# Performance work log

Hardware: AMD Instinct MI355X
Metric: run time of the kernel (lower is better)

Reference implementation:

```python
import jax, jax.numpy as jnp
import numpy as np

DIM_IN, DIM_KEY, HEADS = 1024, 64, 16
B, S = 4, 2048

def setup_inputs() -> dict:
    key = jax.random.key(0)
    ks = jax.random.split(key, 7)
    scale_in = 1.0 / np.sqrt(DIM_IN)
    scale_hd = 1.0 / np.sqrt(HEADS * DIM_KEY)
    return {
        'q_in': jax.random.normal(ks[0], (B, S, DIM_IN), dtype=jnp.float32),
        'k_in': jax.random.normal(ks[1], (B, S, DIM_IN), dtype=jnp.float32),
        'v_in': jax.random.normal(ks[2], (B, S, DIM_IN), dtype=jnp.float32),
        'Wq': jax.random.normal(ks[3], (DIM_IN, HEADS * DIM_KEY), dtype=jnp.float32) * scale_in,
        'Wk': jax.random.normal(ks[4], (DIM_IN, HEADS * DIM_KEY), dtype=jnp.float32) * scale_in,
        'Wv': jax.random.normal(ks[5], (DIM_IN, HEADS * DIM_KEY), dtype=jnp.float32) * scale_in,
        'Wo': jax.random.normal(ks[6], (HEADS * DIM_KEY, DIM_IN), dtype=jnp.float32) * scale_hd,
    }

def reference(q_in, k_in, v_in, Wq, Wk, Wv, Wo):
    b, s, _ = q_in.shape
    def proj(x, W):
        # [B,S,D] @ [D,H*dk] -> [B,H,S,dk]
        return (x @ W).reshape(b, s, HEADS, DIM_KEY).transpose(0, 2, 1, 3)
    q, k, v = proj(q_in, Wq), proj(k_in, Wk), proj(v_in, Wv)
    # scores: [B,H,S,S]; original scales AFTER matmul by 1/sqrt(dim_key)
    score = jnp.einsum('bhqd,bhkd->bhqk', q, k) / jnp.sqrt(jnp.float32(DIM_KEY))
    p = jax.nn.softmax(score, axis=-1)  # dropout is identity in eval mode
    out = jnp.einsum('bhqk,bhkd->bhqd', p, v)
    out = out.transpose(0, 2, 1, 3).reshape(b, s, HEADS * DIM_KEY)
    return out @ Wo
```

## Files before the change

kernel.cpp:

```cpp
#include <hip/hip_runtime.h>
#include <hip/hip_bf16.h>

#define DIN   1024
#define HEADS 16
#define DK    64
#define BATCH 4
#define SEQ   2048
#define MROWS (BATCH*SEQ)
#define HD    (HEADS*DK)

typedef unsigned short u16;
typedef unsigned int   u32;
typedef __attribute__((ext_vector_type(8))) short v8s;
typedef __attribute__((ext_vector_type(4))) float v4f;

__device__ __forceinline__ u16 f2bf(float x) {
  union { float f; u32 u; } v; v.f = x;
  u32 r = v.u + 0x7FFFu + ((v.u >> 16) & 1u);
  return (u16)(r >> 16);
}
__device__ __forceinline__ int cvtpk(float lo, float hi) {
  int r;
  asm("v_cvt_pk_bf16_f32 %0, %1, %2" : "=v"(r) : "v"(lo), "v"(hi));
  return r;
}
__device__ __forceinline__ float max3f(float a, float b, float c) {
  float r;
  asm("v_max3_f32 %0, %1, %2, %3" : "=v"(r) : "v"(a), "v"(b), "v"(c));
  return r;
}
__device__ __forceinline__ void gload16(const void* g, void* l) {
  __builtin_amdgcn_global_load_lds(
      (__attribute__((address_space(1))) void*)(uintptr_t)(g),
      (__attribute__((address_space(3))) void*)(uintptr_t)(l), 16, 0, 0);
}
__device__ __forceinline__ v8s lds_read_swz(const u16* base, int row, int unit) {
  return *(const v8s*)((const char*)base + (row << 7) + (((unit) ^ (row & 7)) << 4));
}

__global__ __launch_bounds__(256) void wtrans4_kernel(
    const float* __restrict__ w0, const float* __restrict__ w1,
    const float* __restrict__ w2, const float* __restrict__ w3,
    u16* __restrict__ o0, u16* __restrict__ o1,
    u16* __restrict__ o2, u16* __restrict__ o3) {
  __shared__ float tile[64][65];
  const float* in = blockIdx.z == 0 ? w0 : blockIdx.z == 1 ? w1 : blockIdx.z == 2 ? w2 : w3;
  u16* out = blockIdx.z == 0 ? o0 : blockIdx.z == 1 ? o1 : blockIdx.z == 2 ? o2 : o3;
  int bx = blockIdx.x * 64;
  int by = blockIdx.y * 64;
  for (int i = threadIdx.x; i < 64 * 64; i += 256) {
    int r = i >> 6, c = i & 63;
    tile[r][c] = in[(size_t)(by + r) * DIN + bx + c];
  }
  __syncthreads();
  for (int i = threadIdx.x; i < 64 * 64; i += 256) {
    int r = i >> 6, c = i & 63;
    out[(size_t)(bx + r) * DIN + by + c] = f2bf(tile[c][r]);
  }
}

__global__ __launch_bounds__(256) void gemm_qkv_kernel(
    const float* __restrict__ q_in, const float* __restrict__ k_in,
    const float* __restrict__ v_in, const u16* __restrict__ Wtq,
    const u16* __restrict__ Wtk, const u16* __restrict__ Wtv,
    u16* __restrict__ Qb, u16* __restrict__ Kb, u16* __restrict__ VtB) {
  __shared__ u16 A_lds[2][128 * 32];
  __shared__ u16 B_lds[2][128 * 32];
  const int which = blockIdx.x >> 9;
  const float* Ain = which == 0 ? q_in : which == 1 ? k_in : v_in;
  const u16* Bt = which == 0 ? Wtq : which == 1 ? Wtk : Wtv;
  u16* Cout = which == 0 ? Qb : which == 1 ? Kb : VtB;

  const int tid = threadIdx.x;
  const int lane = tid & 63;
  const int wv = tid >> 6;
  const int wm = wv & 1, wn = wv >> 1;
  const int bid = blockIdx.x & 511;
  const int swz = (bid & 7) * 64 + (bid >> 3);
  const int m0 = (swz >> 3) * 128;
  const int n0 = (swz & 7) * 128;
  const int l15 = lane & 15;
  const int k8 = (lane >> 4) * 8;

  const float* gaf = Ain + (size_t)(m0 + wv * 16 + (lane >> 2)) * DIN + (lane & 3) * 8;
  const u16* gb = Bt + (size_t)(n0 + wv * 16 + (lane >> 2)) * DIN + (lane & 3) * 8;
  u16* la0 = &A_lds[0][wv * 512 + (lane & 63) * 8];
  u16* la1 = &A_lds[1][wv * 512 + (lane & 63) * 8];

  v4f acc[4][4];
#pragma unroll
  for (int i = 0; i < 4; i++)
#pragma unroll
    for (int j = 0; j < 4; j++) acc[i][j] = (v4f)0.f;

  float4 af0, af1, af2, af3;

#define A_GLOAD(ks)                                                   \
  do {                                                                \
    af0 = ((const float4*)(gaf + (ks) * 32))[0];                      \
    af1 = ((const float4*)(gaf + (ks) * 32))[1];                      \
    af2 = ((const float4*)(gaf + (size_t)64 * DIN + (ks) * 32))[0];   \
    af3 = ((const float4*)(gaf + (size_t)64 * DIN + (ks) * 32))[1];   \
  } while (0)
#define A_DSWRITE(b)                                                  \
  do {                                                                \
    int4 w0 = {cvtpk(af0.x, af0.y), cvtpk(af0.z, af0.w),              \
               cvtpk(af1.x, af1.y), cvtpk(af1.z, af1.w)};             \
    int4 w1 = {cvtpk(af2.x, af2.y), cvtpk(af2.z, af2.w),              \
               cvtpk(af3.x, af3.y), cvtpk(af3.z, af3.w)};             \
    *(int4*)((b) ? la1 : la0) = w0;                                   \
    *(int4*)(((b) ? la1 : la0) + 2048) = w1;                          \
  } while (0)
#define B_STAGE(ks, b)                                                \
  do {                                                                \
    gload16(gb + (ks) * 32, &B_lds[b][wv * 512]);                     \
    gload16(gb + (size_t)64 * DIN + (ks) * 32, &B_lds[b][wv * 512 + 2048]); \
  } while (0)

  A_GLOAD(0);
  A_DSWRITE(0);
  B_STAGE(0, 0);
  __syncthreads();

  for (int ks = 0; ks < 32; ++ks) {
    const int buf = ks & 1;
    v8s a[4], b[4];
#pragma unroll
    for (int mi = 0; mi < 4; mi++)
      a[mi] = *(const v8s*)&A_lds[buf][(wm * 64 + mi * 16 + l15) * 32 + k8];
#pragma unroll
    for (int ni = 0; ni < 4; ni++)
      b[ni] = *(const v8s*)&B_lds[buf][(wn * 64 + ni * 16 + l15) * 32 + k8];
    if (ks < 31) {
      A_GLOAD(ks + 1);
      B_STAGE(ks + 1, buf ^ 1);
    }
    __builtin_amdgcn_s_setprio(1);
#pragma unroll
    for (int mi = 0; mi < 4; mi++)
#pragma unroll
      for (int ni = 0; ni < 4; ni++)
        acc[mi][ni] = __builtin_amdgcn_mfma_f32_16x16x32_bf16(a[mi], b[ni], acc[mi][ni], 0, 0, 0);
    __builtin_amdgcn_s_setprio(0);
    if (ks < 31) A_DSWRITE(buf ^ 1);
    __syncthreads();
  }
#undef A_GLOAD
#undef A_DSWRITE
#undef B_STAGE

  const int grp = lane >> 4;
#pragma unroll
  for (int mi = 0; mi < 4; mi++) {
#pragma unroll
    for (int ni = 0; ni < 4; ni++) {
      int row = m0 + wm * 64 + mi * 16 + grp * 4;
      int col = n0 + wn * 64 + ni * 16 + l15;
      int w01 = cvtpk(acc[mi][ni][0], acc[mi][ni][1]);
      int w23 = cvtpk(acc[mi][ni][2], acc[mi][ni][3]);
      if (which < 2) {
        u16 h[4] = {(u16)w01, (u16)(w01 >> 16), (u16)w23, (u16)(w23 >> 16)};
#pragma unroll
        for (int r = 0; r < 4; r++) {
          int bb = (row + r) >> 11, ss = (row + r) & 2047;
          int hh = col >> 6, dd = col & 63;
          Cout[((((size_t)bb * HEADS + hh) * SEQ + ss) << 6) + dd] = h[r];
        }
      } else {
        int bb = row >> 11, ss = row & 2047;
        int hh = col >> 6, dd = col & 63;
        int2 w = {w01, w23};
        *(int2*)&Cout[((size_t)(bb * HEADS + hh) * DK + dd) * SEQ + ss] = w;
      }
    }
  }
}

__global__ __launch_bounds__(256) void gemm_o_kernel(const u16* __restrict__ A,
                                                     const u16* __restrict__ Bt,
                                                     float* __restrict__ Cout) {
  __shared__ u16 A_lds[2][128 * 32];
  __shared__ u16 B_lds[2][128 * 32];
  const int tid = threadIdx.x;
  const int lane = tid & 63;
  const int wv = tid >> 6;
  const int wm = wv & 1, wn = wv >> 1;
  const int bid = blockIdx.x;
  const int swz = (bid & 7) * 64 + (bid >> 3);
  const int m0 = (swz >> 3) * 128;
  const int n0 = (swz & 7) * 128;
  const int l15 = lane & 15;
  const int k8 = (lane >> 4) * 8;

  const u16* ga = A + (size_t)(m0 + wv * 16 + (lane >> 2)) * DIN + (lane & 3) * 8;
  const u16* gb = Bt + (size_t)(n0 + wv * 16 + (lane >> 2)) * DIN + (lane & 3) * 8;

  v4f acc[4][4];
#pragma unroll
  for (int i = 0; i < 4; i++)
#pragma unroll
    for (int j = 0; j < 4; j++) acc[i][j] = (v4f)0.f;

#define G_STAGE(ks, b)                                              \
  do {                                                              \
    gload16(ga + (ks) * 32, &A_lds[b][wv * 512]);                   \
    gload16(ga + (size_t)64 * DIN + (ks) * 32, &A_lds[b][wv * 512 + 2048]); \
    gload16(gb + (ks) * 32, &B_lds[b][wv * 512]);                   \
    gload16(gb + (size_t)64 * DIN + (ks) * 32, &B_lds[b][wv * 512 + 2048]); \
  } while (0)

  G_STAGE(0, 0);
  __syncthreads();
  for (int ks = 0; ks < 32; ++ks) {
    const int buf = ks & 1;
    v8s a[4], b[4];
#pragma unroll
    for (int mi = 0; mi < 4; mi++)
      a[mi] = *(const v8s*)&A_lds[buf][(wm * 64 + mi * 16 + l15) * 32 + k8];
#pragma unroll
    for (int ni = 0; ni < 4; ni++)
      b[ni] = *(const v8s*)&B_lds[buf][(wn * 64 + ni * 16 + l15) * 32 + k8];
    if (ks < 31) G_STAGE(ks + 1, buf ^ 1);
    __builtin_amdgcn_s_setprio(1);
#pragma unroll
    for (int mi = 0; mi < 4; mi++)
#pragma unroll
      for (int ni = 0; ni < 4; ni++)
        acc[mi][ni] = __builtin_amdgcn_mfma_f32_16x16x32_bf16(a[mi], b[ni], acc[mi][ni], 0, 0, 0);
    __builtin_amdgcn_s_setprio(0);
    __syncthreads();
  }
#undef G_STAGE

  const int grp = lane >> 4;
#pragma unroll
  for (int mi = 0; mi < 4; mi++) {
#pragma unroll
    for (int ni = 0; ni < 4; ni++) {
#pragma unroll
      for (int r = 0; r < 4; r++) {
        int row = m0 + wm * 64 + mi * 16 + grp * 4 + r;
        int col = n0 + wn * 64 + ni * 16 + l15;
        Cout[(size_t)row * HD + col] = acc[mi][ni][r];
      }
    }
  }
}

__global__ __launch_bounds__(512) void attn_kernel(const u16* __restrict__ Q,
                                                   const u16* __restrict__ Kmat,
                                                   const u16* __restrict__ Vt,
                                                   u16* __restrict__ AO) {
  __shared__ u16 K_lds[64 * 64];
  __shared__ u16 V_lds[64 * 64];
  __shared__ u16 P_lds[8][16][72];

  const int tid = threadIdx.x;
  const int lane = tid & 63;
  const int wv = tid >> 6;
  const int l15 = lane & 15;
  const int grp = lane >> 4;
  const int k8 = grp * 8;

  const int bid = blockIdx.x;
  const int swz = (bid & 7) * 128 + (bid >> 3);
  const int bh = swz >> 4;
  const int qt = swz & 15;
  const size_t base = (size_t)bh * SEQ * DK;

  v8s qf[2];
  {
    const int q = qt * 128 + wv * 16 + l15;
    const u16* qp = Q + base + (size_t)q * DK;
    qf[0] = *(const v8s*)(qp + k8);
    qf[1] = *(const v8s*)(qp + 32 + k8);
    const float SCL = 0.125f * 1.44269504f;
#pragma unroll
    for (int j = 0; j < 8; j++) {
      union { float f; u32 u; } a;
      a.u = ((u32)(u16)qf[0][j]) << 16; a.f *= SCL; qf[0][j] = (short)f2bf(a.f);
      a.u = ((u32)(u16)qf[1][j]) << 16; a.f *= SCL; qf[1][j] = (short)f2bf(a.f);
    }
  }

  v8s ones;
#pragma unroll
  for (int j = 0; j < 8; j++) ones[j] = (short)0x3F80;

  float mrow = -1e30f;
  v4f oacc[5];
#pragma unroll
  for (int db = 0; db < 5; db++) oacc[db] = (v4f)0.f;

  const int srow = tid >> 3;
  const int au = tid & 7;
  const int sw = srow & 7;
  const u16* kp_base = Kmat + base + (size_t)srow * DK + au * 8;
  const u16* vp_base = Vt + base + (size_t)srow * SEQ + au * 8;
  u16* krow = &K_lds[srow << 6];
  u16* vrow = &V_lds[srow << 6];

  int4 kr0, vr0;
#define A_LOAD(t)                                                  \
  do {                                                             \
    kr0 = *(const int4*)(kp_base + (size_t)(t) * 64 * DK);         \
    vr0 = *(const int4*)(vp_base + (t) * 64);                      \
  } while (0)
#define A_WRITE()                                                  \
  do {                                                             \
    *(int4*)((char*)krow + ((au ^ sw) << 4)) = kr0;                \
    *(int4*)((char*)vrow + ((au ^ sw) << 4)) = vr0;                \
  } while (0)

  A_LOAD(0);

  for (int t = 0; t < SEQ / 64; ++t) {
    __syncthreads();
    A_WRITE();
    __syncthreads();
    if (t + 1 < SEQ / 64) A_LOAD(t + 1);

    v4f sacc[4];
#pragma unroll
    for (int kb = 0; kb < 4; kb++) sacc[kb] = (v4f)0.f;
    __builtin_amdgcn_s_setprio(1);
#pragma unroll
    for (int ks = 0; ks < 2; ks++)
#pragma unroll
      for (int kb = 0; kb < 4; kb++) {
        v8s kf = lds_read_swz(K_lds, kb * 16 + l15, ks * 4 + grp);
        sacc[kb] = __builtin_amdgcn_mfma_f32_16x16x32_bf16(kf, qf[ks], sacc[kb], 0, 0, 0);
      }
    __builtin_amdgcn_s_setprio(0);

    float m1 = max3f(sacc[0][0], sacc[0][1], sacc[0][2]);
    float m2 = max3f(sacc[0][3], sacc[1][0], sacc[1][1]);
    float m3 = max3f(sacc[1][2], sacc[1][3], sacc[2][0]);
    float m4 = max3f(sacc[2][1], sacc[2][2], sacc[2][3]);
    float m5 = max3f(sacc[3][0], sacc[3][1], sacc[3][2]);
    float mx = fmaxf(max3f(m1, m2, m3), max3f(m4, m5, sacc[3][3]));
    mx = fmaxf(mx, __shfl_xor(mx, 16));
    mx = fmaxf(mx, __shfl_xor(mx, 32));
    if (__any(mx - mrow > 8.f)) {
      float mnew = fmaxf(mrow, mx);
      float fac = __builtin_amdgcn_exp2f(mrow - mnew);
#pragma unroll
      for (int db = 0; db < 5; db++) oacc[db] *= fac;
      mrow = mnew;
    }
    float p[4][4];
#pragma unroll
    for (int kb = 0; kb < 4; kb++)
#pragma unroll
      for (int r = 0; r < 4; r++)
        p[kb][r] = __builtin_amdgcn_exp2f(sacc[kb][r] - mrow);

#pragma unroll
    for (int kb = 0; kb < 4; kb++) {
      int2 w;
      w.x = cvtpk(p[kb][0], p[kb][1]);
      w.y = cvtpk(p[kb][2], p[kb][3]);
      *(int2*)&P_lds[wv][l15][kb * 16 + grp * 4] = w;
    }
    asm volatile("s_waitcnt lgkmcnt(0)" ::: "memory");

    __builtin_amdgcn_s_setprio(1);
#pragma unroll
    for (int ks = 0; ks < 2; ks++) {
      v8s pf = *(const v8s*)&P_lds[wv][l15][ks * 32 + k8];
#pragma unroll
      for (int db = 0; db < 4; db++) {
        v8s vf = lds_read_swz(V_lds, db * 16 + l15, ks * 4 + grp);
        oacc[db] = __builtin_amdgcn_mfma_f32_16x16x32_bf16(vf, pf, oacc[db], 0, 0, 0);
      }
      oacc[4] = __builtin_amdgcn_mfma_f32_16x16x32_bf16(ones, pf, oacc[4], 0, 0, 0);
    }
    __builtin_amdgcn_s_setprio(0);
  }
#undef A_LOAD
#undef A_WRITE

  const int bb = bh >> 4, hh = bh & 15;
  const int q = qt * 128 + wv * 16 + l15;
  const float inv = 1.0f / oacc[4][0];
  const size_t rowbase = ((size_t)bb * SEQ + q) * HD + hh * DK;
#pragma unroll
  for (int db = 0; db < 4; db++) {
    int2 w;
    w.x = cvtpk(oacc[db][0] * inv, oacc[db][1] * inv);
    w.y = cvtpk(oacc[db][2] * inv, oacc[db][3] * inv);
    *(int2*)&AO[rowbase + db * 16 + grp * 4] = w;
  }
}

extern "C" void kernel_launch(void* const* d_in, const int* in_sizes, int n_in,
                              void* d_out, int out_size, void* d_ws, size_t ws_size,
                              hipStream_t stream) {
  const float* q_in = (const float*)d_in[0];
  const float* k_in = (const float*)d_in[1];
  const float* v_in = (const float*)d_in[2];
  const float* Wq = (const float*)d_in[3];
  const float* Wk = (const float*)d_in[4];
  const float* Wv = (const float*)d_in[5];
  const float* Wo = (const float*)d_in[6];
  float* out = (float*)d_out;

  u16* ws = (u16*)d_ws;
  const size_t M1 = (size_t)1 << 20;
  u16* Wtq = ws;
  u16* Wtk = Wtq + M1;
  u16* Wtv = Wtk + M1;
  u16* Wto = Wtv + M1;
  u16* Qb = Wto + M1;
  u16* Kb = Qb + (size_t)MROWS * HD;
  u16* VtB = Kb + (size_t)MROWS * HD;
  u16* AO = VtB + (size_t)MROWS * HD;

  dim3 tb(256);
  wtrans4_kernel<<<dim3(16, 16, 4), tb, 0, stream>>>(Wq, Wk, Wv, Wo, Wtq, Wtk, Wtv, Wto);

  gemm_qkv_kernel<<<dim3(1536), tb, 0, stream>>>(q_in, k_in, v_in,
                                                 Wtq, Wtk, Wtv, Qb, Kb, VtB);

  attn_kernel<<<dim3(1024), dim3(512), 0, stream>>>(Qb, Kb, VtB, AO);

  gemm_o_kernel<<<dim3(512), tb, 0, stream>>>(AO, Wto, out);
}
```

Baseline: 199.8 us.

## Switch attention to 32x32x16 MFMA with register-resident P via permlane32 swap

The attention kernel now uses 4 waves (256 threads) per block, each owning 32 query rows, and computes S and O with 32x32x16 bf16 MFMAs instead of 16x16x32. The P tile no longer goes through LDS: it is converted to bf16 and rearranged in registers with v_permlane32_swap so it can feed the PV MFMA directly. The softmax row sum is accumulated in registers rather than with an extra ones-vector MFMA. The aim is to cut LDS round-trips and extra MFMAs per tile, at the cost of more registers per wave and fewer waves per block for hiding latency.

```diff
diff --git a/kernel.cpp b/kernel.cpp
--- a/kernel.cpp
+++ b/kernel.cpp
@@ -13,6 +13,7 @@
 typedef unsigned int   u32;
 typedef __attribute__((ext_vector_type(8))) short v8s;
 typedef __attribute__((ext_vector_type(4))) float v4f;
+typedef __attribute__((ext_vector_type(16))) float v16f;
 
 __device__ __forceinline__ u16 f2bf(float x) {
   union { float f; u32 u; } v; v.f = x;
@@ -247,20 +248,18 @@
   }
 }
 
-__global__ __launch_bounds__(512) void attn_kernel(const u16* __restrict__ Q,
+__global__ __launch_bounds__(256) void attn_kernel(const u16* __restrict__ Q,
                                                    const u16* __restrict__ Kmat,
                                                    const u16* __restrict__ Vt,
                                                    u16* __restrict__ AO) {
   __shared__ u16 K_lds[64 * 64];
   __shared__ u16 V_lds[64 * 64];
-  __shared__ u16 P_lds[8][16][72];
 
   const int tid = threadIdx.x;
   const int lane = tid & 63;
   const int wv = tid >> 6;
-  const int l15 = lane & 15;
-  const int grp = lane >> 4;
-  const int k8 = grp * 8;
+  const int l31 = lane & 31;
+  const int h = lane >> 5;
 
   const int bid = blockIdx.x;
   const int swz = (bid & 7) * 128 + (bid >> 3);
@@ -268,48 +267,51 @@
   const int qt = swz & 15;
   const size_t base = (size_t)bh * SEQ * DK;
 
-  v8s qf[2];
+  v8s qf[4];
   {
-    const int q = qt * 128 + wv * 16 + l15;
-    const u16* qp = Q + base + (size_t)q * DK;
-    qf[0] = *(const v8s*)(qp + k8);
-    qf[1] = *(const v8s*)(qp + 32 + k8);
+    const int q = qt * 128 + wv * 32 + l31;
+    const u16* qp = Q + base + (size_t)q * DK + h * 8;
     const float SCL = 0.125f * 1.44269504f;
 #pragma unroll
-    for (int j = 0; j < 8; j++) {
-      union { float f; u32 u; } a;
-      a.u = ((u32)(u16)qf[0][j]) << 16; a.f *= SCL; qf[0][j] = (short)f2bf(a.f);
-      a.u = ((u32)(u16)qf[1][j]) << 16; a.f *= SCL; qf[1][j] = (short)f2bf(a.f);
-    }
-  }
-
-  v8s ones;
-#pragma unroll
-  for (int j = 0; j < 8; j++) ones[j] = (short)0x3F80;
-
-  float mrow = -1e30f;
-  v4f oacc[5];
-#pragma unroll
-  for (int db = 0; db < 5; db++) oacc[db] = (v4f)0.f;
-
-  const int srow = tid >> 3;
-  const int au = tid & 7;
+    for (int ks = 0; ks < 4; ks++) {
+      qf[ks] = *(const v8s*)(qp + ks * 16);
+#pragma unroll
+      for (int j = 0; j < 8; j++) {
+        union { float f; u32 u; } a;
+        a.u = ((u32)(u16)qf[ks][j]) << 16; a.f *= SCL; qf[ks][j] = (short)f2bf(a.f);
+      }
+    }
+  }
+
+  float mrow = -1e30f, lrow = 0.f;
+  v16f oacc[2];
+  oacc[0] = (v16f)0.f;
+  oacc[1] = (v16f)0.f;
+
+  const int srow = tid >> 2;
+  const int a3 = tid & 3;
   const int sw = srow & 7;
-  const u16* kp_base = Kmat + base + (size_t)srow * DK + au * 8;
-  const u16* vp_base = Vt + base + (size_t)srow * SEQ + au * 8;
+  const u16* kp_base = Kmat + base + (size_t)srow * DK + a3 * 16;
+  const u16* vp_base = Vt + base + (size_t)srow * SEQ + a3 * 16;
   u16* krow = &K_lds[srow << 6];
   u16* vrow = &V_lds[srow << 6];
 
-  int4 kr0, vr0;
+  int4 kr0, kr1, vr0, vr1;
 #define A_LOAD(t)                                                  \
   do {                                                             \
-    kr0 = *(const int4*)(kp_base + (size_t)(t) * 64 * DK);         \
-    vr0 = *(const int4*)(vp_base + (t) * 64);                      \
+    const u16* kp = kp_base + (size_t)(t) * 64 * DK;               \
+    const u16* vp = vp_base + (t) * 64;                            \
+    kr0 = ((const int4*)kp)[0];                                    \
+    kr1 = ((const int4*)kp)[1];                                    \
+    vr0 = ((const int4*)vp)[0];                                    \
+    vr1 = ((const int4*)vp)[1];                                    \
   } while (0)
 #define A_WRITE()                                                  \
   do {                                                             \
-    *(int4*)((char*)krow + ((au ^ sw) << 4)) = kr0;                \
-    *(int4*)((char*)vrow + ((au ^ sw) << 4)) = vr0;                \
+    *(int4*)((char*)krow + (((2 * a3 + 0) ^ sw) << 4)) = kr0;      \
+    *(int4*)((char*)krow + (((2 * a3 + 1) ^ sw) << 4)) = kr1;      \
+    *(int4*)((char*)vrow + (((2 * a3 + 0) ^ sw) << 4)) = vr0;      \
+    *(int4*)((char*)vrow + (((2 * a3 + 1) ^ sw) << 4)) = vr1;      \
   } while (0)
 
   A_LOAD(0);
@@ -320,77 +322,95 @@
     __syncthreads();
     if (t + 1 < SEQ / 64) A_LOAD(t + 1);
 
-    v4f sacc[4];
-#pragma unroll
-    for (int kb = 0; kb < 4; kb++) sacc[kb] = (v4f)0.f;
+    v16f sacc[2];
+    sacc[0] = (v16f)0.f;
+    sacc[1] = (v16f)0.f;
     __builtin_amdgcn_s_setprio(1);
 #pragma unroll
-    for (int ks = 0; ks < 2; ks++)
-#pragma unroll
-      for (int kb = 0; kb < 4; kb++) {
-        v8s kf = lds_read_swz(K_lds, kb * 16 + l15, ks * 4 + grp);
-        sacc[kb] = __builtin_amdgcn_mfma_f32_16x16x32_bf16(kf, qf[ks], sacc[kb], 0, 0, 0);
+    for (int ks = 0; ks < 4; ks++)
+#pragma unroll
+      for (int kb = 0; kb < 2; kb++) {
+        v8s kf = lds_read_swz(K_lds, kb * 32 + l31, ks * 2 + h);
+        sacc[kb] = __builtin_amdgcn_mfma_f32_32x32x16_bf16(kf, qf[ks], sacc[kb], 0, 0, 0);
       }
     __builtin_amdgcn_s_setprio(0);
 
-    float m1 = max3f(sacc[0][0], sacc[0][1], sacc[0][2]);
-    float m2 = max3f(sacc[0][3], sacc[1][0], sacc[1][1]);
-    float m3 = max3f(sacc[1][2], sacc[1][3], sacc[2][0]);
-    float m4 = max3f(sacc[2][1], sacc[2][2], sacc[2][3]);
-    float m5 = max3f(sacc[3][0], sacc[3][1], sacc[3][2]);
-    float mx = fmaxf(max3f(m1, m2, m3), max3f(m4, m5, sacc[3][3]));
-    mx = fmaxf(mx, __shfl_xor(mx, 16));
+    float a0 = max3f(sacc[0][0], sacc[0][1], sacc[0][2]);
+    float a1 = max3f(sacc[0][3], sacc[0][4], sacc[0][5]);
+    float a2 = max3f(sacc[0][6], sacc[0][7], sacc[0][8]);
+    float a3m = max3f(sacc[0][9], sacc[0][10], sacc[0][11]);
+    float a4 = max3f(sacc[0][12], sacc[0][13], sacc[0][14]);
+    float a5 = max3f(sacc[1][0], sacc[1][1], sacc[1][2]);
+    float a6 = max3f(sacc[1][3], sacc[1][4], sacc[1][5]);
+    float a7 = max3f(sacc[1][6], sacc[1][7], sacc[1][8]);
+    float a8 = max3f(sacc[1][9], sacc[1][10], sacc[1][11]);
+    float a9 = max3f(sacc[1][12], sacc[1][13], sacc[1][14]);
+    float b0 = max3f(a0, a1, a2);
+    float b1 = max3f(a3m, a4, sacc[0][15]);
+    float b2 = max3f(a5, a6, a7);
+    float b3 = max3f(a8, a9, sacc[1][15]);
+    float mx = fmaxf(fmaxf(b0, b1), fmaxf(b2, b3));
     mx = fmaxf(mx, __shfl_xor(mx, 32));
     if (__any(mx - mrow > 8.f)) {
       float mnew = fmaxf(mrow, mx);
       float fac = __builtin_amdgcn_exp2f(mrow - mnew);
 #pragma unroll
-      for (int db = 0; db < 5; db++) oacc[db] *= fac;
+      for (int i = 0; i < 16; i++) { oacc[0][i] *= fac; oacc[1][i] *= fac; }
+      lrow *= fac;
       mrow = mnew;
     }
-    float p[4][4];
-#pragma unroll
-    for (int kb = 0; kb < 4; kb++)
-#pragma unroll
-      for (int r = 0; r < 4; r++)
-        p[kb][r] = __builtin_amdgcn_exp2f(sacc[kb][r] - mrow);
-
-#pragma unroll
-    for (int kb = 0; kb < 4; kb++) {
-      int2 w;
-      w.x = cvtpk(p[kb][0], p[kb][1]);
-      w.y = cvtpk(p[kb][2], p[kb][3]);
-      *(int2*)&P_lds[wv][l15][kb * 16 + grp * 4] = w;
-    }
-    asm volatile("s_waitcnt lgkmcnt(0)" ::: "memory");
+    float ls = 0.f;
+#pragma unroll
+    for (int kb = 0; kb < 2; kb++)
+#pragma unroll
+      for (int i = 0; i < 16; i++) {
+        sacc[kb][i] = __builtin_amdgcn_exp2f(sacc[kb][i] - mrow);
+        ls += sacc[kb][i];
+      }
+    ls += __shfl_xor(ls, 32);
+    lrow += ls;
 
     __builtin_amdgcn_s_setprio(1);
 #pragma unroll
-    for (int ks = 0; ks < 2; ks++) {
-      v8s pf = *(const v8s*)&P_lds[wv][l15][ks * 32 + k8];
-#pragma unroll
-      for (int db = 0; db < 4; db++) {
-        v8s vf = lds_read_swz(V_lds, db * 16 + l15, ks * 4 + grp);
-        oacc[db] = __builtin_amdgcn_mfma_f32_16x16x32_bf16(vf, pf, oacc[db], 0, 0, 0);
-      }
-      oacc[4] = __builtin_amdgcn_mfma_f32_16x16x32_bf16(ones, pf, oacc[4], 0, 0, 0);
-    }
+    for (int kb = 0; kb < 2; kb++)
+#pragma unroll
+      for (int s = 0; s < 2; s++) {
+        int T0 = cvtpk(sacc[kb][8 * s + 0], sacc[kb][8 * s + 1]);
+        int T1 = cvtpk(sacc[kb][8 * s + 2], sacc[kb][8 * s + 3]);
+        int T2 = cvtpk(sacc[kb][8 * s + 4], sacc[kb][8 * s + 5]);
+        int T3 = cvtpk(sacc[kb][8 * s + 6], sacc[kb][8 * s + 7]);
+        asm("v_permlane32_swap_b32 %0, %1" : "+v"(T0), "+v"(T2));
+        asm("v_permlane32_swap_b32 %0, %1" : "+v"(T1), "+v"(T3));
+        union { int4 i; v8s s8; } pw;
+        pw.i.x = T0;
+        pw.i.y = T1;
+        pw.i.z = T2;
+        pw.i.w = T3;
+        const int st = kb * 2 + s;
+#pragma unroll
+        for (int db = 0; db < 2; db++) {
+          v8s vf = lds_read_swz(V_lds, db * 32 + l31, st * 2 + h);
+          oacc[db] = __builtin_amdgcn_mfma_f32_32x32x16_bf16(vf, pw.s8, oacc[db], 0, 0, 0);
+        }
+      }
     __builtin_amdgcn_s_setprio(0);
   }
 #undef A_LOAD
 #undef A_WRITE
 
   const int bb = bh >> 4, hh = bh & 15;
-  const int q = qt * 128 + wv * 16 + l15;
-  const float inv = 1.0f / oacc[4][0];
+  const int q = qt * 128 + wv * 32 + l31;
+  const float inv = 1.0f / lrow;
   const size_t rowbase = ((size_t)bb * SEQ + q) * HD + hh * DK;
 #pragma unroll
-  for (int db = 0; db < 4; db++) {
-    int2 w;
-    w.x = cvtpk(oacc[db][0] * inv, oacc[db][1] * inv);
-    w.y = cvtpk(oacc[db][2] * inv, oacc[db][3] * inv);
-    *(int2*)&AO[rowbase + db * 16 + grp * 4] = w;
-  }
+  for (int db = 0; db < 2; db++)
+#pragma unroll
+    for (int g = 0; g < 4; g++) {
+      int2 w;
+      w.x = cvtpk(oacc[db][4 * g + 0] * inv, oacc[db][4 * g + 1] * inv);
+      w.y = cvtpk(oacc[db][4 * g + 2] * inv, oacc[db][4 * g + 3] * inv);
+      *(int2*)&AO[rowbase + db * 32 + g * 8 + h * 4] = w;
+    }
 }
 
 extern "C" void kernel_launch(void* const* d_in, const int* in_sizes, int n_in,
@@ -422,7 +442,7 @@
   gemm_qkv_kernel<<<dim3(1536), tb, 0, stream>>>(q_in, k_in, v_in,
                                                  Wtq, Wtk, Wtv, Qb, Kb, VtB);
 
-  attn_kernel<<<dim3(1024), dim3(512), 0, stream>>>(Qb, Kb, VtB, AO);
+  attn_kernel<<<dim3(1024), tb, 0, stream>>>(Qb, Kb, VtB, AO);
 
   gemm_o_kernel<<<dim3(512), tb, 0, stream>>>(AO, Wto, out);
 }
```

After: 205.5 us. 2.8% more time.
